# Kernel tuning notes

Hardware: AMD Instinct MI355X
Metric: run time of the kernel (lower is better)

Reference implementation:

```python
import jax, jax.numpy as jnp
import numpy as np

B, H, W, DIM = 8, 64, 64, 256
HEADS, DH = 8, 64
HID = HEADS * DH  # 512
EPS = 1e-5


def setup_inputs() -> dict:
    key = jax.random.key(0)
    k0, k1, k2 = jax.random.split(key, 3)
    return {
        "x": jax.random.normal(k0, (B, H, W, DIM), dtype=jnp.float32),
        "w_qkv": jax.random.normal(k1, (DIM, 3 * HID), dtype=jnp.float32) / np.sqrt(DIM),
        "gn_scale": jnp.ones((HID,), jnp.float32),
        "gn_bias": jnp.zeros((HID,), jnp.float32),
        "w_out": jax.random.normal(k2, (HID, DIM), dtype=jnp.float32) / np.sqrt(HID),
        "b_out": jnp.zeros((DIM,), jnp.float32),
    }


def reference(x, w_qkv, gn_scale, gn_bias, w_out, b_out):
    b, h, w, c = x.shape
    n = h * w
    scale = DH ** -0.5
    # 1x1 conv (no bias) == channel matmul
    qkv = jnp.einsum('bxyc,cf->bxyf', x, w_qkv)
    q, k, v = jnp.split(qkv, 3, axis=-1)
    # 'b x y (h c) -> b h c (x y)'
    to_heads = lambda t: t.reshape(b, n, HEADS, DH).transpose(0, 2, 3, 1)
    q, k, v = map(to_heads, (q, k, v))  # [b, heads, d, n]
    q = jax.nn.softmax(q, axis=-2) * scale  # softmax over feature dim d
    k = jax.nn.softmax(k, axis=-1)          # softmax over token dim n
    context = jnp.einsum('bhdn,bhen->bhde', k, v)   # small d x e context
    out = jnp.einsum('bhde,bhdn->bhen', context, q)  # [b, heads, e, n]
    # 'b h c (x y) -> b x y (h c)'
    out = out.transpose(0, 3, 1, 2).reshape(b, h, w, HID)
    # GroupNorm with 1 group: normalize over (H, W, C) per sample
    mu = out.mean(axis=(1, 2, 3), keepdims=True)
    var = out.var(axis=(1, 2, 3), keepdims=True)
    out = (out - mu) * jax.lax.rsqrt(var + EPS) * gn_scale + gn_bias
    # final 1x1 conv with bias
    return jnp.einsum('bxyf,fc->bxyc', out, w_out) + b_out
```

## Files before the change

### kernel.cpp

```cpp
#include <hip/hip_runtime.h>


typedef unsigned short ushort_t;
typedef __attribute__((ext_vector_type(8))) short short8;
typedef __attribute__((ext_vector_type(4))) float floatx4;

__device__ __forceinline__ float b2f(ushort_t u) {
  unsigned int i = ((unsigned int)u) << 16;
  float f;
  __builtin_memcpy(&f, &i, 4);
  return f;
}
__device__ __forceinline__ ushort_t f2b(float f) {
  unsigned int i;
  __builtin_memcpy(&i, &f, 4);
  unsigned int r = (i + 0x7FFFu + ((i >> 16) & 1u)) >> 16;
  return (ushort_t)r;
}

__device__ __forceinline__ void load_lds16(const ushort_t* g, ushort_t* l) {
  __builtin_amdgcn_global_load_lds(
      (const __attribute__((address_space(1))) unsigned int*)g,
      (__attribute__((address_space(3))) unsigned int*)l, 16, 0, 0);
}

__global__ __launch_bounds__(256) void cast_f32_bf16(
    const float* __restrict__ in, ushort_t* __restrict__ out) {
  long i = ((long)blockIdx.x * 256 + threadIdx.x) * 4;
  float4 v = *(const float4*)(in + i);
  ushort4 o;
  o.x = f2b(v.x);
  o.y = f2b(v.y);
  o.z = f2b(v.z);
  o.w = f2b(v.w);
  *(ushort4*)(out + i) = o;
}

__global__ __launch_bounds__(256) void transpose_f32_bf16(
    const float* __restrict__ in, ushort_t* __restrict__ out, int R, int C,
    const float* __restrict__ scale) {
  __shared__ ushort_t t[32][33];
  int c0 = blockIdx.x * 32, r0 = blockIdx.y * 32;
  int tx = threadIdx.x & 31, ty = threadIdx.x >> 5;
  for (int i = 0; i < 32; i += 8) {
    float s = scale ? scale[r0 + ty + i] : 1.0f;
    t[ty + i][tx] = f2b(in[(long)(r0 + ty + i) * C + c0 + tx] * s);
  }
  __syncthreads();
  for (int i = 0; i < 32; i += 8)
    out[(long)(c0 + ty + i) * R + r0 + tx] = t[tx][ty + i];
}

__global__ __launch_bounds__(64) void prep_gw_kernel(
    const float* __restrict__ gn_scale, const float* __restrict__ gn_bias,
    const float* __restrict__ w_out, const float* __restrict__ b_out,
    float* __restrict__ gw1, float* __restrict__ bias2) {
  int c = blockIdx.x * 64 + threadIdx.x;
  float g1 = 0.f, b2 = 0.f;
  for (int f = 0; f < 512; ++f) {
    float w = w_out[f * 256 + c];
    g1 += gn_scale[f] * w;
    b2 += gn_bias[f] * w;
  }
  gw1[c] = g1;
  bias2[c] = b2 + b_out[c];
}

template <int MODE, bool SWAP>
__global__ __launch_bounds__(256) void gemm_tpl(
    const ushort_t* __restrict__ A, const ushort_t* __restrict__ Bt,
    void* __restrict__ Cv, int M, int K, int F,
    const float* __restrict__ murs, const float* __restrict__ gw1,
    const float* __restrict__ bias2) {
  __shared__ __align__(16) ushort_t As[128][32];
  __shared__ __align__(16) ushort_t Bs[128][32];
  int tid = threadIdx.x;
  long m0 = (long)(SWAP ? blockIdx.y : blockIdx.x) * 128;
  long f0 = (long)(SWAP ? blockIdx.x : blockIdx.y) * 128;
  int wv = tid >> 6, lane = tid & 63;
  int wm = wv & 1, wf = wv >> 1;
  int l15 = lane & 15, quad = lane >> 4;

  floatx4 acc[4][4];
  floatx4 zero = {0.f, 0.f, 0.f, 0.f};
  for (int i = 0; i < 4; i++)
    for (int j = 0; j < 4; j++) acc[i][j] = zero;

  for (int k0 = 0; k0 < K; k0 += 32) {
    __syncthreads();
#pragma unroll
    for (int r = 0; r < 2; ++r) {
      int chunk = r * 256 + tid;
      int row = chunk >> 2;
      int kc = chunk & 3;
      load_lds16(A + (m0 + row) * (long)K + k0 + kc * 8, &As[row][kc * 8]);
      load_lds16(Bt + (f0 + row) * (long)K + k0 + kc * 8, &Bs[row][kc * 8]);
    }
    __syncthreads();
    short8 af[4], bfr[4];
#pragma unroll
    for (int mt = 0; mt < 4; mt++)
      af[mt] = *(const short8*)(&As[wm * 64 + mt * 16 + l15][quad * 8]);
#pragma unroll
    for (int ft = 0; ft < 4; ft++)
      bfr[ft] = *(const short8*)(&Bs[wf * 64 + ft * 16 + l15][quad * 8]);
#pragma unroll
    for (int mt = 0; mt < 4; mt++)
#pragma unroll
      for (int ft = 0; ft < 4; ft++)
        acc[mt][ft] = __builtin_amdgcn_mfma_f32_16x16x32_bf16(
            af[mt], bfr[ft], acc[mt][ft], 0, 0, 0);
  }

  if constexpr (MODE == 1) {
    ushort_t* C = (ushort_t*)Cv;
    bool isk = (m0 < 512);
#pragma unroll
    for (int mt = 0; mt < 4; mt++)
#pragma unroll
      for (int ft = 0; ft < 4; ft++) {
        long col = f0 + wf * 64 + ft * 16 + l15;
#pragma unroll
        for (int r = 0; r < 4; r++) {
          long row = m0 + wm * 64 + mt * 16 + quad * 4 + r;
          float v = acc[mt][ft][r];
          if (isk) v = __expf(v);
          C[row * F + col] = f2b(v);
        }
      }
  } else {
    float* C = (float*)Cv;
    int b = (int)(m0 >> 12);
    float mu = murs[b * 2], rs = murs[b * 2 + 1];
#pragma unroll
    for (int mt = 0; mt < 4; mt++)
#pragma unroll
      for (int ft = 0; ft < 4; ft++) {
        long col = f0 + wf * 64 + ft * 16 + l15;
        float c1 = bias2[col] - rs * mu * gw1[col];
#pragma unroll
        for (int r = 0; r < 4; r++) {
          long row = m0 + wm * 64 + mt * 16 + quad * 4 + r;
          C[row * F + col] = rs * acc[mt][ft][r] + c1;
        }
      }
  }
}

__global__ __launch_bounds__(256) void ctx_mfma(
    const ushort_t* __restrict__ kvT, float* __restrict__ ctxP,
    float* __restrict__ ksumP) {
  int bh = blockIdx.x, cy = blockIdx.y;
  int b = bh >> 3, h = bh & 7;
  int tid = threadIdx.x, wv = tid >> 6, lane = tid & 63;
  int l15 = lane & 15, quad = lane >> 4;
  __shared__ __align__(16) ushort_t kTs[64 * 128];
  __shared__ __align__(16) ushort_t vTs[64 * 128];
  const ushort_t* kbase = kvT + (long)(h * 64) * 32768 + b * 4096 + cy * 256;
  const ushort_t* vbase = kbase + (long)512 * 32768;

  floatx4 acc[4], acc1;
  floatx4 zero = {0.f, 0.f, 0.f, 0.f};
  for (int i = 0; i < 4; i++) acc[i] = zero;
  acc1 = zero;
  short8 ones;
#pragma unroll
  for (int u = 0; u < 8; ++u) ones[u] = (short)0x3F80;

  int r4 = lane >> 4, c = lane & 15;
  for (int tile = 0; tile < 2; ++tile) {
    __syncthreads();
#pragma unroll
    for (int i = 0; i < 4; ++i) {
      int row = wv * 16 + i * 4 + r4;
      int gc = (c & 8) | ((c ^ row) & 7);
      load_lds16(kbase + (long)row * 32768 + tile * 128 + gc * 8,
                 kTs + (wv * 16 + i * 4) * 128 + lane * 8);
      load_lds16(vbase + (long)row * 32768 + tile * 128 + gc * 8,
                 vTs + (wv * 16 + i * 4) * 128 + lane * 8);
    }
    __syncthreads();
#pragma unroll
    for (int ks = 0; ks < 4; ++ks) {
      int d = wv * 16 + l15;
      int cidx = ks * 4 + quad;
      int sa = (cidx & 8) | ((cidx ^ d) & 7);
      short8 a = *(const short8*)(kTs + d * 128 + sa * 8);
      short8 bf[4];
#pragma unroll
      for (int ft = 0; ft < 4; ++ft) {
        int e = ft * 16 + l15;
        int sb = (cidx & 8) | ((cidx ^ e) & 7);
        bf[ft] = *(const short8*)(vTs + e * 128 + sb * 8);
      }
#pragma unroll
      for (int ft = 0; ft < 4; ++ft)
        acc[ft] = __builtin_amdgcn_mfma_f32_16x16x32_bf16(a, bf[ft], acc[ft],
                                                          0, 0, 0);
      acc1 = __builtin_amdgcn_mfma_f32_16x16x32_bf16(a, ones, acc1, 0, 0, 0);
    }
  }
  float* cb = ctxP + ((long)cy * 64 + bh) * 4096;
#pragma unroll
  for (int ft = 0; ft < 4; ++ft)
#pragma unroll
    for (int r = 0; r < 4; ++r)
      cb[(ft * 16 + l15) * 64 + wv * 16 + quad * 4 + r] = acc[ft][r];
  if (l15 == 0) {
    float* kb = ksumP + ((long)cy * 64 + bh) * 64;
#pragma unroll
    for (int r = 0; r < 4; ++r) kb[wv * 16 + quad * 4 + r] = acc1[r];
  }
}

__global__ __launch_bounds__(256) void reduce_kernel(
    const float* __restrict__ ctxP, const float* __restrict__ ksumP,
    ushort_t* __restrict__ ctxB) {
  int bid = blockIdx.x;
  int bh = bid >> 4;
  int j = (bid & 15) * 256 + threadIdx.x;
  int e = j >> 6, d = j & 63;
  float ks = 0.f;
#pragma unroll
  for (int c = 0; c < 16; ++c) ks += ksumP[((long)c * 64 + bh) * 64 + d];
  float s = 0.f;
#pragma unroll
  for (int c = 0; c < 16; ++c) s += ctxP[((long)c * 64 + bh) * 4096 + j];
  int slot = (d >> 3) ^ (e & 7);
  ctxB[(long)bh * 4096 + e * 64 + slot * 8 + (d & 7)] = f2b(s / ks);
}

__global__ __launch_bounds__(256) void qattn_kernel(
    const ushort_t* __restrict__ xb, const ushort_t* __restrict__ wqT,
    const ushort_t* __restrict__ ctxB, ushort_t* __restrict__ A2,
    float* __restrict__ gstats) {
  __shared__ __align__(16) char lds[49216];
  ushort_t* As = (ushort_t*)lds;
  ushort_t* Bs = (ushort_t*)(lds + 8192);
  ushort_t* P = (ushort_t*)lds;
  ushort_t* Cs = (ushort_t*)(lds + 32768);
  float* red = (float*)(lds + 49152);

  int tid = threadIdx.x;
  int bx = blockIdx.x, by = blockIdx.y;
  long m0 = (long)bx * 128;
  long f0 = (long)by * 128;
  int wv = tid >> 6, lane = tid & 63;
  int wm = wv & 1, wf = wv >> 1;
  int l15 = lane & 15, quad = lane >> 4;
  int b = bx >> 5;

  floatx4 acc[4][4];
  floatx4 zero = {0.f, 0.f, 0.f, 0.f};
  for (int i = 0; i < 4; i++)
    for (int j = 0; j < 4; j++) acc[i][j] = zero;

  for (int k0 = 0; k0 < 256; k0 += 32) {
    __syncthreads();
#pragma unroll
    for (int r = 0; r < 2; ++r) {
      int chunk = r * 256 + tid;
      int row = chunk >> 2;
      int kc = chunk & 3;
      load_lds16(xb + (m0 + row) * 256 + k0 + kc * 8, As + row * 32 + kc * 8);
      load_lds16(wqT + (f0 + row) * 256 + k0 + kc * 8, Bs + row * 32 + kc * 8);
    }
    __syncthreads();
    short8 af[4], bfr[4];
#pragma unroll
    for (int mt = 0; mt < 4; mt++)
      af[mt] = *(const short8*)(As + (wm * 64 + mt * 16 + l15) * 32 + quad * 8);
#pragma unroll
    for (int ft = 0; ft < 4; ft++)
      bfr[ft] =
          *(const short8*)(Bs + (wf * 64 + ft * 16 + l15) * 32 + quad * 8);
#pragma unroll
    for (int mt = 0; mt < 4; mt++)
#pragma unroll
      for (int ft = 0; ft < 4; ft++)
        acc[mt][ft] = __builtin_amdgcn_mfma_f32_16x16x32_bf16(
            af[mt], bfr[ft], acc[mt][ft], 0, 0, 0);
  }
  __syncthreads();

  {
    const ushort_t* cg = ctxB + ((long)(b * 8 + by * 2)) * 4096;
#pragma unroll
    for (int i = 0; i < 4; ++i)
      load_lds16(cg + (i * 4 + wv) * 512 + lane * 8,
                 Cs + (i * 4 + wv) * 512 + lane * 8);
  }

  float rs[4][4];
#pragma unroll
  for (int mt = 0; mt < 4; mt++)
#pragma unroll
    for (int r = 0; r < 4; r++) rs[mt][r] = 0.f;
#pragma unroll
  for (int mt = 0; mt < 4; mt++)
#pragma unroll
    for (int ft = 0; ft < 4; ft++)
#pragma unroll
      for (int r = 0; r < 4; r++) {
        float e = __expf(acc[mt][ft][r]);
        acc[mt][ft][r] = e;
        rs[mt][r] += e;
      }
#pragma unroll
  for (int mt = 0; mt < 4; mt++)
#pragma unroll
    for (int r = 0; r < 4; r++) {
      float t = rs[mt][r];
      t += __shfl_xor(t, 1);
      t += __shfl_xor(t, 2);
      t += __shfl_xor(t, 4);
      t += __shfl_xor(t, 8);
      rs[mt][r] = 0.125f / t;
    }

  {
    ushort_t* Pw = P + wf * 8192;
#pragma unroll
    for (int mt = 0; mt < 4; mt++)
#pragma unroll
      for (int ft = 0; ft < 4; ft++) {
        int d = ft * 16 + l15;
#pragma unroll
        for (int r = 0; r < 4; r++) {
          int row = wm * 64 + mt * 16 + quad * 4 + r;
          int slot = (d >> 3) ^ (row & 7);
          Pw[row * 64 + slot * 8 + (d & 7)] = f2b(acc[mt][ft][r]);
        }
      }
  }
  __syncthreads();

  floatx4 o[4][4];
  for (int i = 0; i < 4; i++)
    for (int j = 0; j < 4; j++) o[i][j] = zero;
  {
    const ushort_t* Pr = P + wf * 8192;
    const ushort_t* Cr = Cs + wf * 4096;
#pragma unroll
    for (int k0 = 0; k0 < 2; ++k0) {
      short8 af[4], bfr[4];
#pragma unroll
      for (int mt = 0; mt < 4; mt++) {
        int row = wm * 64 + mt * 16 + l15;
        int slot = (k0 * 4 + quad) ^ (row & 7);
        af[mt] = *(const short8*)(Pr + row * 64 + slot * 8);
      }
#pragma unroll
      for (int ft = 0; ft < 4; ft++) {
        int e = ft * 16 + l15;
        int slot = (k0 * 4 + quad) ^ (e & 7);
        bfr[ft] = *(const short8*)(Cr + e * 64 + slot * 8);
      }
#pragma unroll
      for (int mt = 0; mt < 4; mt++)
#pragma unroll
        for (int ft = 0; ft < 4; ft++)
          o[mt][ft] = __builtin_amdgcn_mfma_f32_16x16x32_bf16(af[mt], bfr[ft],
                                                              o[mt][ft], 0, 0,
                                                              0);
    }
  }

  float lsum = 0.f, lss = 0.f;
#pragma unroll
  for (int mt = 0; mt < 4; mt++)
#pragma unroll
    for (int ft = 0; ft < 4; ft++) {
      long col = f0 + wf * 64 + ft * 16 + l15;
#pragma unroll
      for (int r = 0; r < 4; r++) {
        long row = m0 + wm * 64 + mt * 16 + quad * 4 + r;
        float v = o[mt][ft][r] * rs[mt][r];
        A2[row * 512 + col] = f2b(v);
        lsum += v;
        lss += v * v;
      }
    }
  for (int s = 32; s > 0; s >>= 1) {
    lsum += __shfl_xor(lsum, s);
    lss += __shfl_xor(lss, s);
  }
  if (lane == 0) {
    red[wv * 2] = lsum;
    red[wv * 2 + 1] = lss;
  }
  __syncthreads();
  if (tid == 0) {
    float a = 0.f, c = 0.f;
    for (int w2 = 0; w2 < 4; w2++) {
      a += red[w2 * 2];
      c += red[w2 * 2 + 1];
    }
    atomicAdd(&gstats[b * 2], a);
    atomicAdd(&gstats[b * 2 + 1], c);
  }
}

__global__ __launch_bounds__(64) void finalize_murs(
    const float* __restrict__ gstats, float* __restrict__ murs) {
  int tid = threadIdx.x;
  if (tid < 8) {
    float cnt = 4096.f * 512.f;
    float mu = gstats[tid * 2] / cnt;
    float var = gstats[tid * 2 + 1] / cnt - mu * mu;
    murs[tid * 2] = mu;
    murs[tid * 2 + 1] = rsqrtf(var + 1e-5f);
  }
}

extern "C" void kernel_launch(void* const* d_in, const int* in_sizes, int n_in,
                              void* d_out, int out_size, void* d_ws,
                              size_t ws_size, hipStream_t stream) {
  const float* x = (const float*)d_in[0];
  const float* w_qkv = (const float*)d_in[1];
  const float* gn_scale = (const float*)d_in[2];
  const float* gn_bias = (const float*)d_in[3];
  const float* w_out = (const float*)d_in[4];
  const float* b_out = (const float*)d_in[5];
  float* out = (float*)d_out;

  char* w = (char*)d_ws;
  ushort_t* kvT = (ushort_t*)(w + 33554432);
  ushort_t* A2 = (ushort_t*)(w + 100663296);
  float* ctxP = (float*)(w + 134217728);
  float* ksumP = (float*)(w + 150994944);
  ushort_t* xb = (ushort_t*)(w + 167772160);
  ushort_t* wqkvT = (ushort_t*)(w + 184549376);
  ushort_t* w2T = (ushort_t*)(w + 185335808);
  ushort_t* ctxB = (ushort_t*)(w + 185630720);
  float* gstats = (float*)(w + 186679296);
  float* murs = (float*)(w + 186695744);
  float* bias2 = (float*)(w + 186695808);
  float* gw1 = (float*)(w + 186696832);

  hipMemsetAsync(gstats, 0, 64, stream);

  cast_f32_bf16<<<8388608 / 4 / 256, 256, 0, stream>>>(x, xb);
  transpose_f32_bf16<<<dim3(1536 / 32, 256 / 32), 256, 0, stream>>>(
      w_qkv, wqkvT, 256, 1536, nullptr);
  transpose_f32_bf16<<<dim3(256 / 32, 512 / 32), 256, 0, stream>>>(
      w_out, w2T, 512, 256, gn_scale);
  prep_gw_kernel<<<4, 64, 0, stream>>>(gn_scale, gn_bias, w_out, b_out, gw1,
                                       bias2);
  gemm_tpl<1, true><<<dim3(256, 8), 256, 0, stream>>>(
      wqkvT + 512 * 256, xb, kvT, 1024, 256, 32768, nullptr, nullptr, nullptr);
  ctx_mfma<<<dim3(64, 16), 256, 0, stream>>>(kvT, ctxP, ksumP);
  reduce_kernel<<<1024, 256, 0, stream>>>(ctxP, ksumP, ctxB);
  qattn_kernel<<<dim3(256, 4), 256, 0, stream>>>(xb, wqkvT, ctxB, A2, gstats);
  finalize_murs<<<1, 64, 0, stream>>>(gstats, murs);
  gemm_tpl<2, false><<<dim3(256, 2), 256, 0, stream>>>(
      A2, w2T, out, 32768, 512, 256, murs, gw1, bias2);
}
```

Before: 236.5 us.

## Widen q-GEMM K-step to 64 with swizzled LDS, load context directly to registers

The q-projection GEMM in qattn_kernel now stages 64-wide K tiles with an XOR-swizzled LDS layout, which halves the number of barrier-separated load phases. The context matrix is read straight from global memory into registers instead of being staged through LDS. The softmax normalisation is folded into P before it is stored. Together these cut LDS from about 48KB to 32KB and add a launch bound of 4 blocks per SM, aiming for higher occupancy and fewer syncs. The cost is more register pressure from the extra context fragments, and the intra-wave ordering of P writes and reads after the removed barrier must stay correct.

```diff
diff --git a/kernel.cpp b/kernel.cpp
--- a/kernel.cpp
+++ b/kernel.cpp
@@ -230,16 +230,15 @@
   ctxB[(long)bh * 4096 + e * 64 + slot * 8 + (d & 7)] = f2b(s / ks);
 }
 
-__global__ __launch_bounds__(256) void qattn_kernel(
+__global__ __launch_bounds__(256, 4) void qattn_kernel(
     const ushort_t* __restrict__ xb, const ushort_t* __restrict__ wqT,
     const ushort_t* __restrict__ ctxB, ushort_t* __restrict__ A2,
     float* __restrict__ gstats) {
-  __shared__ __align__(16) char lds[49216];
+  __shared__ __align__(16) char lds[32800];
   ushort_t* As = (ushort_t*)lds;
-  ushort_t* Bs = (ushort_t*)(lds + 8192);
+  ushort_t* Bs = (ushort_t*)(lds + 16384);
   ushort_t* P = (ushort_t*)lds;
-  ushort_t* Cs = (ushort_t*)(lds + 32768);
-  float* red = (float*)(lds + 49152);
+  float* red = (float*)(lds + 32768);
 
   int tid = threadIdx.x;
   int bx = blockIdx.x, by = blockIdx.y;
@@ -255,41 +254,52 @@
   for (int i = 0; i < 4; i++)
     for (int j = 0; j < 4; j++) acc[i][j] = zero;
 
-  for (int k0 = 0; k0 < 256; k0 += 32) {
-    __syncthreads();
-#pragma unroll
-    for (int r = 0; r < 2; ++r) {
+  for (int k0 = 0; k0 < 256; k0 += 64) {
+    __syncthreads();
+#pragma unroll
+    for (int r = 0; r < 4; ++r) {
       int chunk = r * 256 + tid;
-      int row = chunk >> 2;
-      int kc = chunk & 3;
-      load_lds16(xb + (m0 + row) * 256 + k0 + kc * 8, As + row * 32 + kc * 8);
-      load_lds16(wqT + (f0 + row) * 256 + k0 + kc * 8, Bs + row * 32 + kc * 8);
-    }
-    __syncthreads();
-    short8 af[4], bfr[4];
-#pragma unroll
-    for (int mt = 0; mt < 4; mt++)
-      af[mt] = *(const short8*)(As + (wm * 64 + mt * 16 + l15) * 32 + quad * 8);
-#pragma unroll
-    for (int ft = 0; ft < 4; ft++)
-      bfr[ft] =
-          *(const short8*)(Bs + (wf * 64 + ft * 16 + l15) * 32 + quad * 8);
-#pragma unroll
-    for (int mt = 0; mt < 4; mt++)
-#pragma unroll
-      for (int ft = 0; ft < 4; ft++)
-        acc[mt][ft] = __builtin_amdgcn_mfma_f32_16x16x32_bf16(
-            af[mt], bfr[ft], acc[mt][ft], 0, 0, 0);
-  }
+      int row = chunk >> 3;
+      int kc = chunk & 7;
+      int gc = kc ^ (row & 7);
+      load_lds16(xb + (m0 + row) * 256 + k0 + gc * 8, As + chunk * 8);
+      load_lds16(wqT + (f0 + row) * 256 + k0 + gc * 8, Bs + chunk * 8);
+    }
+    __syncthreads();
+#pragma unroll
+    for (int ks = 0; ks < 2; ++ks) {
+      short8 af[4], bfr[4];
+#pragma unroll
+      for (int mt = 0; mt < 4; mt++) {
+        int row = wm * 64 + mt * 16 + l15;
+        int slot = (ks * 4 + quad) ^ (row & 7);
+        af[mt] = *(const short8*)(As + row * 64 + slot * 8);
+      }
+#pragma unroll
+      for (int ft = 0; ft < 4; ft++) {
+        int rowb = wf * 64 + ft * 16 + l15;
+        int slot = (ks * 4 + quad) ^ (rowb & 7);
+        bfr[ft] = *(const short8*)(Bs + rowb * 64 + slot * 8);
+      }
+#pragma unroll
+      for (int mt = 0; mt < 4; mt++)
+#pragma unroll
+        for (int ft = 0; ft < 4; ft++)
+          acc[mt][ft] = __builtin_amdgcn_mfma_f32_16x16x32_bf16(
+              af[mt], bfr[ft], acc[mt][ft], 0, 0, 0);
+    }
+  }
+
+  const ushort_t* cg = ctxB + ((long)(b * 8 + by * 2 + wf)) * 4096;
+  short8 cfr0[4];
+#pragma unroll
+  for (int ft = 0; ft < 4; ++ft) {
+    int e = ft * 16 + l15;
+    int slot = quad ^ (e & 7);
+    cfr0[ft] = *(const short8*)(cg + e * 64 + slot * 8);
+  }
+
   __syncthreads();
-
-  {
-    const ushort_t* cg = ctxB + ((long)(b * 8 + by * 2)) * 4096;
-#pragma unroll
-    for (int i = 0; i < 4; ++i)
-      load_lds16(cg + (i * 4 + wv) * 512 + lane * 8,
-                 Cs + (i * 4 + wv) * 512 + lane * 8);
-  }
 
   float rs[4][4];
 #pragma unroll
@@ -329,41 +339,51 @@
         for (int r = 0; r < 4; r++) {
           int row = wm * 64 + mt * 16 + quad * 4 + r;
           int slot = (d >> 3) ^ (row & 7);
-          Pw[row * 64 + slot * 8 + (d & 7)] = f2b(acc[mt][ft][r]);
+          Pw[row * 64 + slot * 8 + (d & 7)] = f2b(acc[mt][ft][r] * rs[mt][r]);
         }
       }
   }
-  __syncthreads();
+
+  short8 cfr1[4];
+#pragma unroll
+  for (int ft = 0; ft < 4; ++ft) {
+    int e = ft * 16 + l15;
+    int slot = (4 + quad) ^ (e & 7);
+    cfr1[ft] = *(const short8*)(cg + e * 64 + slot * 8);
+  }
 
   floatx4 o[4][4];
   for (int i = 0; i < 4; i++)
     for (int j = 0; j < 4; j++) o[i][j] = zero;
   {
     const ushort_t* Pr = P + wf * 8192;
-    const ushort_t* Cr = Cs + wf * 4096;
-#pragma unroll
-    for (int k0 = 0; k0 < 2; ++k0) {
-      short8 af[4], bfr[4];
-#pragma unroll
-      for (int mt = 0; mt < 4; mt++) {
-        int row = wm * 64 + mt * 16 + l15;
-        int slot = (k0 * 4 + quad) ^ (row & 7);
-        af[mt] = *(const short8*)(Pr + row * 64 + slot * 8);
-      }
-#pragma unroll
-      for (int ft = 0; ft < 4; ft++) {
-        int e = ft * 16 + l15;
-        int slot = (k0 * 4 + quad) ^ (e & 7);
-        bfr[ft] = *(const short8*)(Cr + e * 64 + slot * 8);
-      }
-#pragma unroll
-      for (int mt = 0; mt < 4; mt++)
-#pragma unroll
-        for (int ft = 0; ft < 4; ft++)
-          o[mt][ft] = __builtin_amdgcn_mfma_f32_16x16x32_bf16(af[mt], bfr[ft],
-                                                              o[mt][ft], 0, 0,
-                                                              0);
-    }
+    short8 af[4];
+#pragma unroll
+    for (int mt = 0; mt < 4; mt++) {
+      int row = wm * 64 + mt * 16 + l15;
+      int slot = quad ^ (row & 7);
+      af[mt] = *(const short8*)(Pr + row * 64 + slot * 8);
+    }
+#pragma unroll
+    for (int mt = 0; mt < 4; mt++)
+#pragma unroll
+      for (int ft = 0; ft < 4; ft++)
+        o[mt][ft] = __builtin_amdgcn_mfma_f32_16x16x32_bf16(af[mt], cfr0[ft],
+                                                            o[mt][ft], 0, 0,
+                                                            0);
+#pragma unroll
+    for (int mt = 0; mt < 4; mt++) {
+      int row = wm * 64 + mt * 16 + l15;
+      int slot = (4 + quad) ^ (row & 7);
+      af[mt] = *(const short8*)(Pr + row * 64 + slot * 8);
+    }
+#pragma unroll
+    for (int mt = 0; mt < 4; mt++)
+#pragma unroll
+      for (int ft = 0; ft < 4; ft++)
+        o[mt][ft] = __builtin_amdgcn_mfma_f32_16x16x32_bf16(af[mt], cfr1[ft],
+                                                            o[mt][ft], 0, 0,
+                                                            0);
   }
 
   float lsum = 0.f, lss = 0.f;
@@ -375,7 +395,7 @@
 #pragma unroll
       for (int r = 0; r < 4; r++) {
         long row = m0 + wm * 64 + mt * 16 + quad * 4 + r;
-        float v = o[mt][ft][r] * rs[mt][r];
+        float v = o[mt][ft][r];
         A2[row * 512 + col] = f2b(v);
         lsum += v;
         lss += v * v;
```

Measured after the change: 240.5 us. No clear change (+1.7%).
